# Kernel tuning notes

Measured on AMD Instinct MI355X. Metric: run time of the kernel, lower is better.

Reference implementation:

```python
import jax, jax.numpy as jnp
import numpy as np

C = 256      # n_embd
H = 16       # n_head
HS = C // H  # head_size = 16
B = 64
T = 256      # <= block_size
LN_EPS = 1e-5


def _layer_norm(x, g, b):
    mu = jnp.mean(x, axis=-1, keepdims=True)
    var = jnp.mean((x - mu) ** 2, axis=-1, keepdims=True)
    return (x - mu) * jax.lax.rsqrt(var + LN_EPS) * g + b


def setup_inputs() -> dict:
    key = jax.random.key(0)
    ks = jax.random.split(key, 10)
    s_in = 1.0 / np.sqrt(C)
    s_ff = 1.0 / np.sqrt(4 * C)
    return {
        "x": jax.random.normal(ks[0], (B, T, C), dtype=jnp.float32),
        # per-head Q/K/V weights, stacked: [H, C, HS] (no bias, as in Head)
        "Wq": jax.random.normal(ks[1], (H, C, HS), dtype=jnp.float32) * s_in,
        "Wk": jax.random.normal(ks[2], (H, C, HS), dtype=jnp.float32) * s_in,
        "Wv": jax.random.normal(ks[3], (H, C, HS), dtype=jnp.float32) * s_in,
        "Wp": jax.random.normal(ks[4], (C, C), dtype=jnp.float32) * s_in,
        "bp": jnp.zeros((C,), dtype=jnp.float32),
        "W1": jax.random.normal(ks[5], (C, 4 * C), dtype=jnp.float32) * s_in,
        "b1": jnp.zeros((4 * C,), dtype=jnp.float32),
        "W2": jax.random.normal(ks[6], (4 * C, C), dtype=jnp.float32) * s_ff,
        "b2": jnp.zeros((C,), dtype=jnp.float32),
        "g1": jnp.ones((C,), dtype=jnp.float32),
        "be1": jnp.zeros((C,), dtype=jnp.float32),
        "g2": jnp.ones((C,), dtype=jnp.float32),
        "be2": jnp.zeros((C,), dtype=jnp.float32),
    }


def reference(x, Wq, Wk, Wv, Wp, bp, W1, b1, W2, b2, g1, be1, g2, be2):
    Bx, Tx, Cx = x.shape
    h = _layer_norm(x, g1, be1)
    # per-head projections: [B, H, T, HS]
    q = jnp.einsum('btc,hcd->bhtd', h, Wq)
    k = jnp.einsum('btc,hcd->bhtd', h, Wk)
    v = jnp.einsum('btc,hcd->bhtd', h, Wv)
    # NOTE: original scales by C**-0.5 with C = n_embd, NOT head_size
    scale = 1.0 / np.sqrt(Cx)
    scores = jnp.einsum('bhtd,bhsd->bhts', q, k) * scale
    causal = jnp.tril(jnp.ones((Tx, Tx), dtype=bool))
    scores = jnp.where(causal, scores, -jnp.inf)
    wei = jax.nn.softmax(scores, axis=-1)  # dropout = identity (eval)
    attn = jnp.einsum('bhts,bhsd->bhtd', wei, v)
    # concat heads in order -> [B, T, C]
    attn = attn.transpose(0, 2, 1, 3).reshape(Bx, Tx, Cx)
    attn = attn @ Wp + bp
    x = x + attn
    h2 = _layer_norm(x, g2, be2)
    ffn = jax.nn.gelu(h2 @ W1 + b1, approximate=False) @ W2 + b2
    return x + ffn


if __name__ == "__main__":
    out = reference(**setup_inputs())
    print(out.shape, out.dtype)
```

## Files before the change

kernel.cpp:

```cpp
#include <hip/hip_runtime.h>
#include <hip/hip_bf16.h>

typedef __attribute__((ext_vector_type(8))) short short8;
typedef __attribute__((ext_vector_type(4))) float f32x4;
typedef __attribute__((ext_vector_type(16))) float f32x16;

__device__ __forceinline__ unsigned short f2bf(float f) {
    unsigned u = __float_as_uint(f);
    unsigned r = (u + 0x7fffu + ((u >> 16) & 1u)) >> 16;
    return (unsigned short)r;
}

__device__ __forceinline__ float fast_gelu(float v) {
    float y  = 0.7978845608f * v * (1.0f + 0.044715f * v * v);
    float ay = fabsf(y);
    float e  = __expf(2.0f * ay);
    float th = 1.0f - 2.0f / (e + 1.0f);
    th = __builtin_copysignf(th, y);
    return 0.5f * v * (1.0f + th);
}

__device__ __forceinline__ void gload16(const unsigned short* g, unsigned short* l) {
    __builtin_amdgcn_global_load_lds(
        (const __attribute__((address_space(1))) unsigned int*)g,
        (__attribute__((address_space(3))) unsigned int*)l,
        16, 0, 0);
}

__global__ __launch_bounds__(256) void prep_ln1(
    const float* __restrict__ Wq, const float* __restrict__ Wk,
    const float* __restrict__ Wv, const float* __restrict__ Wp,
    const float* __restrict__ W1, const float* __restrict__ W2,
    unsigned short* __restrict__ WqkvT, unsigned short* __restrict__ WpT,
    unsigned short* __restrict__ W1T, unsigned short* __restrict__ W2T,
    const float* __restrict__ xin, const float* __restrict__ gw,
    const float* __restrict__ bw, unsigned short* __restrict__ h1)
{
    __shared__ float smem[4096];
    const int bid = blockIdx.x, t = threadIdx.x;
    if (bid >= 624) {
        int row  = (bid - 624) * 4 + (t >> 6);
        int lane = t & 63;
        const float4 v = *reinterpret_cast<const float4*>(xin + (size_t)row * 256 + lane * 4);
        float s  = v.x + v.y + v.z + v.w;
        float sq = v.x*v.x + v.y*v.y + v.z*v.z + v.w*v.w;
#pragma unroll
        for (int m = 1; m < 64; m <<= 1) { s += __shfl_xor(s, m); sq += __shfl_xor(sq, m); }
        float mean = s * (1.0f/256.0f);
        float var  = sq * (1.0f/256.0f) - mean*mean;
        float rstd = rsqrtf(var + 1e-5f);
        const float4 g4 = *reinterpret_cast<const float4*>(gw + lane*4);
        const float4 b4 = *reinterpret_cast<const float4*>(bw + lane*4);
        ushort4 o;
        o.x = f2bf((v.x-mean)*rstd*g4.x + b4.x);
        o.y = f2bf((v.y-mean)*rstd*g4.y + b4.y);
        o.z = f2bf((v.z-mean)*rstd*g4.z + b4.z);
        o.w = f2bf((v.w-mean)*rstd*g4.w + b4.w);
        *reinterpret_cast<ushort4*>(h1 + (size_t)row*256 + lane*4) = o;
        return;
    }
    if (bid < 576) {
        const float* W; unsigned short* WT; int N, K, tile0;
        if (bid < 64)       { W = Wp; WT = WpT; N = 256;  K = 256;  tile0 = bid; }
        else if (bid < 320) { W = W1; WT = W1T; N = 1024; K = 256;  tile0 = bid - 64; }
        else                { W = W2; WT = W2T; N = 256;  K = 1024; tile0 = bid - 320; }
        int ntx = N >> 5;
        int bx = tile0 % ntx, by = tile0 / ntx;
        int c0 = bx*32, r0 = by*32;
        int tx = t & 31, ty = t >> 5;
#pragma unroll
        for (int i = 0; i < 4; ++i)
            smem[(ty + i*8)*33 + tx] = W[(size_t)(r0 + ty + i*8)*N + c0 + tx];
        __syncthreads();
#pragma unroll
        for (int i = 0; i < 4; ++i)
            WT[(size_t)(c0 + ty + i*8)*K + r0 + tx] = f2bf(smem[tx*33 + ty + i*8]);
    } else {
        int pb = bid - 576;
        int proj = pb >> 4, hh = pb & 15;
        const float* W = (proj == 0) ? Wq : ((proj == 1) ? Wk : Wv);
        float scale = (proj == 0) ? 0.0625f : 1.0f;
        const float4* src = reinterpret_cast<const float4*>(W + hh*4096);
#pragma unroll
        for (int i = 0; i < 4; ++i) {
            float4 v4 = src[t + i*256];
            *reinterpret_cast<float4*>(&smem[(t + i*256)*4]) = v4;
        }
        __syncthreads();
        int d = t >> 4, cp = (t & 15) * 16;
        unsigned short obuf[16];
#pragma unroll
        for (int i = 0; i < 16; ++i)
            obuf[i] = f2bf(smem[(cp + i)*16 + d] * scale);
        unsigned short* dst = WqkvT + (size_t)(proj*256 + hh*16 + d)*256 + cp;
        *reinterpret_cast<ushort4*>(dst)      = *reinterpret_cast<ushort4*>(&obuf[0]);
        *reinterpret_cast<ushort4*>(dst + 4)  = *reinterpret_cast<ushort4*>(&obuf[4]);
        *reinterpret_cast<ushort4*>(dst + 8)  = *reinterpret_cast<ushort4*>(&obuf[8]);
        *reinterpret_cast<ushort4*>(dst + 12) = *reinterpret_cast<ushort4*>(&obuf[12]);
    }
}

template<int NBX>
__device__ __forceinline__ void swz_bid(int& bx, int& by) {
    int nwg = gridDim.x;
    int bid = blockIdx.x;
    int vid = (bid & 7) * (nwg >> 3) + (bid >> 3);
    bx = vid % NBX;
    by = vid / NBX;
}

template<int BM, int BN, int K>
__device__ __forceinline__ void gemm_core(
    const unsigned short* __restrict__ A, const unsigned short* __restrict__ BT,
    int bx, int by, f32x4 (&acc)[BM/32][BN/32])
{
    constexpr int FM = BM/32, FN = BN/32, NT = K/32;
    __shared__ unsigned short As[2][BM*32];
    __shared__ unsigned short Bs[2][BN*32];
    const int tid = threadIdx.x, lane = tid & 63, wid = tid >> 6;
    const int wr = (wid >> 1) * (BM/2), wc = (wid & 1) * (BN/2);
    const int c16 = lane & 15, g16 = lane >> 4;
    const int lr = lane >> 2, lq = lane & 3;

#pragma unroll
    for (int m = 0; m < FM; ++m)
#pragma unroll
        for (int n = 0; n < FN; ++n) acc[m][n] = f32x4{0.f, 0.f, 0.f, 0.f};

    const unsigned short* a0 = A  + (size_t)(by*BM + lr)*K + lq*8;
    const unsigned short* b0 = BT + (size_t)(bx*BN + lr)*K + lq*8;

    auto stage = [&](int buf, int t) {
        int k0 = t * 32;
#pragma unroll
        for (int i = 0; i < BM/64; ++i) {
            int ch = wid*(BM/64) + i;
            gload16(a0 + (size_t)ch*16*K + k0, &As[buf][ch*512]);
        }
#pragma unroll
        for (int i = 0; i < BN/64; ++i) {
            int ch = wid*(BN/64) + i;
            gload16(b0 + (size_t)ch*16*K + k0, &Bs[buf][ch*512]);
        }
    };

    auto compute = [&](int buf) {
        short8 af[FM], bf[FN];
#pragma unroll
        for (int m = 0; m < FM; ++m)
            af[m] = *reinterpret_cast<const short8*>(&As[buf][(wr + m*16 + c16)*32 + g16*8]);
#pragma unroll
        for (int n = 0; n < FN; ++n)
            bf[n] = *reinterpret_cast<const short8*>(&Bs[buf][(wc + n*16 + c16)*32 + g16*8]);
#pragma unroll
        for (int m = 0; m < FM; ++m)
#pragma unroll
            for (int n = 0; n < FN; ++n)
                acc[m][n] = __builtin_amdgcn_mfma_f32_16x16x32_bf16(af[m], bf[n], acc[m][n], 0, 0, 0);
    };

    stage(0, 0);
    __syncthreads();
    int cur = 0;
    for (int t = 0; t < NT-1; ++t) {
        stage(cur ^ 1, t + 1);
        compute(cur);
        __syncthreads();
        cur ^= 1;
    }
    compute(cur);
}

template<int BM, int BN, int K>
__device__ __forceinline__ void gemm_core8(
    const unsigned short* __restrict__ A, const unsigned short* __restrict__ BT,
    int by, f32x4 (&acc)[BM/32][BN/64])
{
    constexpr int FM = BM/32, FN = BN/64, NT = K/32;
    constexpr int NCHA = BM/16, NCH = BM/16 + BN/16;
    constexpr int NR = (NCH + 7) / 8;
    __shared__ unsigned short As[2][BM*32];
    __shared__ unsigned short Bs[2][BN*32];
    const int tid = threadIdx.x, lane = tid & 63, wid = tid >> 6;
    const int wm = wid >> 2, wn = wid & 3;
    const int c16 = lane & 15, g16 = lane >> 4;
    const int lr = lane >> 2, lq = lane & 3;

#pragma unroll
    for (int m = 0; m < FM; ++m)
#pragma unroll
        for (int n = 0; n < FN; ++n) acc[m][n] = f32x4{0.f, 0.f, 0.f, 0.f};

    const unsigned short* a0 = A  + (size_t)(by*BM + lr)*K + lq*8;
    const unsigned short* b0 = BT + (size_t)lr*K + lq*8;

    auto stage = [&](int buf, int t) {
        int k0 = t * 32;
#pragma unroll
        for (int i = 0; i < NR; ++i) {
            int ch = i*8 + wid;
            if (ch < NCHA)
                gload16(a0 + (size_t)ch*16*K + k0, &As[buf][ch*512]);
            else if (ch < NCH)
                gload16(b0 + (size_t)(ch-NCHA)*16*K + k0, &Bs[buf][(ch-NCHA)*512]);
        }
    };

    auto compute = [&](int buf) {
        short8 af[FM], bf[FN];
#pragma unroll
        for (int m = 0; m < FM; ++m)
            af[m] = *reinterpret_cast<const short8*>(&As[buf][(wm*(BM/2) + m*16 + c16)*32 + g16*8]);
#pragma unroll
        for (int n = 0; n < FN; ++n)
            bf[n] = *reinterpret_cast<const short8*>(&Bs[buf][(wn*(BN/4) + n*16 + c16)*32 + g16*8]);
#pragma unroll
        for (int m = 0; m < FM; ++m)
#pragma unroll
            for (int n = 0; n < FN; ++n)
                acc[m][n] = __builtin_amdgcn_mfma_f32_16x16x32_bf16(af[m], bf[n], acc[m][n], 0, 0, 0);
    };

    stage(0, 0);
    __syncthreads();
    int cur = 0;
    for (int t = 0; t < NT-1; ++t) {
        stage(cur ^ 1, t + 1);
        compute(cur);
        __syncthreads();
        cur ^= 1;
    }
    compute(cur);
}

__global__ __launch_bounds__(256) void gemm_qkv(
    const unsigned short* __restrict__ A, const unsigned short* __restrict__ BT,
    unsigned short* __restrict__ qb, unsigned short* __restrict__ kb,
    unsigned short* __restrict__ vtb)
{
    int bx, by; swz_bid<6>(bx, by);
    f32x4 acc[4][4];
    gemm_core<128, 128, 256>(A, BT, bx, by, acc);
    const int lane = threadIdx.x & 63, wid = threadIdx.x >> 6;
    const int c16 = lane & 15, g16 = lane >> 4;
    const int wr = (wid >> 1) * 64, wc = (wid & 1) * 64;
#pragma unroll
    for (int m = 0; m < 4; ++m)
#pragma unroll
    for (int n = 0; n < 4; ++n)
#pragma unroll
    for (int j = 0; j < 4; ++j) {
        int row = by*128 + wr + m*16 + g16*4 + j;
        int col = bx*128 + wc + n*16 + c16;
        int proj = col >> 8, hh = (col >> 4) & 15, dd = col & 15;
        int b = row >> 8, t = row & 255;
        unsigned short val = f2bf(acc[m][n][j]);
        size_t bh = (size_t)(b*16 + hh);
        if (proj == 0)      qb[(bh*256 + t)*16 + dd] = val;
        else if (proj == 1) kb[(bh*256 + t)*16 + dd] = val;
        else                vtb[(bh*16 + dd)*256 + t] = val;
    }
}

__global__ __launch_bounds__(512) void gemm_wp_ln(
    const unsigned short* __restrict__ A, const unsigned short* __restrict__ BT,
    const float* __restrict__ bp, const float* __restrict__ x,
    const float* __restrict__ g2, const float* __restrict__ be2,
    float* __restrict__ x2, unsigned short* __restrict__ h2)
{
    int bx, by; swz_bid<1>(bx, by);
    f32x4 acc[2][4];
    gemm_core8<64, 256, 256>(A, BT, by, acc);

    __shared__ float rs[64][4];
    __shared__ float rq[64][4];
    const int tid = threadIdx.x, lane = tid & 63, wid = tid >> 6;
    const int c16 = lane & 15, g16 = lane >> 4;
    const int wm = wid >> 2, wn = wid & 3;

    float vv[2][4][4];
#pragma unroll
    for (int m = 0; m < 2; ++m)
#pragma unroll
    for (int n = 0; n < 4; ++n)
#pragma unroll
    for (int j = 0; j < 4; ++j) {
        int row = by*64 + wm*32 + m*16 + g16*4 + j;
        int col = wn*64 + n*16 + c16;
        size_t idx = (size_t)row*256 + col;
        float v = acc[m][n][j] + bp[col] + x[idx];
        vv[m][n][j] = v;
        x2[idx] = v;
    }
#pragma unroll
    for (int m = 0; m < 2; ++m)
#pragma unroll
    for (int j = 0; j < 4; ++j) {
        float ps = vv[m][0][j] + vv[m][1][j] + vv[m][2][j] + vv[m][3][j];
        float pq = vv[m][0][j]*vv[m][0][j] + vv[m][1][j]*vv[m][1][j]
                 + vv[m][2][j]*vv[m][2][j] + vv[m][3][j]*vv[m][3][j];
#pragma unroll
        for (int mask = 1; mask < 16; mask <<= 1) {
            ps += __shfl_xor(ps, mask);
            pq += __shfl_xor(pq, mask);
        }
        if (c16 == 0) {
            int r = wm*32 + m*16 + g16*4 + j;
            rs[r][wn] = ps;
            rq[r][wn] = pq;
        }
    }
    __syncthreads();
#pragma unroll
    for (int m = 0; m < 2; ++m)
#pragma unroll
    for (int j = 0; j < 4; ++j) {
        int r = wm*32 + m*16 + g16*4 + j;
        float s = rs[r][0] + rs[r][1] + rs[r][2] + rs[r][3];
        float q = rq[r][0] + rq[r][1] + rq[r][2] + rq[r][3];
        float mean = s * (1.0f/256.0f);
        float var  = q * (1.0f/256.0f) - mean*mean;
        float rstd = rsqrtf(var + 1e-5f);
        int row = by*64 + r;
#pragma unroll
        for (int n = 0; n < 4; ++n) {
            int col = wn*64 + n*16 + c16;
            h2[(size_t)row*256 + col] = f2bf((vv[m][n][j]-mean)*rstd*g2[col] + be2[col]);
        }
    }
}

__global__ __launch_bounds__(256) void gemm_ffn1(
    const unsigned short* __restrict__ A, const unsigned short* __restrict__ BT,
    const float* __restrict__ b1, unsigned short* __restrict__ ffh)
{
    int bx, by; swz_bid<8>(bx, by);
    f32x4 acc[4][4];
    gemm_core<128, 128, 256>(A, BT, bx, by, acc);
    const int lane = threadIdx.x & 63, wid = threadIdx.x >> 6;
    const int c16 = lane & 15, g16 = lane >> 4;
    const int wr = (wid >> 1) * 64, wc = (wid & 1) * 64;
#pragma unroll
    for (int m = 0; m < 4; ++m)
#pragma unroll
    for (int n = 0; n < 4; ++n)
#pragma unroll
    for (int j = 0; j < 4; ++j) {
        int row = by*128 + wr + m*16 + g16*4 + j;
        int col = bx*128 + wc + n*16 + c16;
        float v = acc[m][n][j] + b1[col];
        ffh[(size_t)row*1024 + col] = f2bf(fast_gelu(v));
    }
}

__global__ __launch_bounds__(512) void gemm_ffn2(
    const unsigned short* __restrict__ A, const unsigned short* __restrict__ BT,
    const float* __restrict__ b2, const float* __restrict__ x2, float* __restrict__ out)
{
    int bx, by; swz_bid<1>(bx, by);
    f32x4 acc[2][4];
    gemm_core8<64, 256, 1024>(A, BT, by, acc);
    const int lane = threadIdx.x & 63, wid = threadIdx.x >> 6;
    const int c16 = lane & 15, g16 = lane >> 4;
    const int wm = wid >> 2, wn = wid & 3;
#pragma unroll
    for (int m = 0; m < 2; ++m)
#pragma unroll
    for (int n = 0; n < 4; ++n)
#pragma unroll
    for (int j = 0; j < 4; ++j) {
        int row = by*64 + wm*32 + m*16 + g16*4 + j;
        int col = wn*64 + n*16 + c16;
        size_t idx = (size_t)row*256 + col;
        out[idx] = acc[m][n][j] + b2[col] + x2[idx];
    }
}

__global__ __launch_bounds__(256) void attn_kernel(
    const unsigned short* __restrict__ qb, const unsigned short* __restrict__ kb,
    const unsigned short* __restrict__ vtb, unsigned short* __restrict__ ao)
{
    const int bid  = blockIdx.x;
    const int half = bid & 1, h = (bid >> 1) & 15, b = bid >> 5;
    const int tid  = threadIdx.x;
    const int w    = tid >> 6, lane = tid & 63;
    const int l31  = lane & 31, hi = lane >> 5;
    const int chunk = half*4 + w;
    const int t0    = chunk * 32;
    const unsigned short* qh = qb  + (size_t)(b*16 + h) * 4096;
    const unsigned short* kh = kb  + (size_t)(b*16 + h) * 4096;
    const unsigned short* vh = vtb + (size_t)(b*16 + h) * 4096;

    short8 qf = *reinterpret_cast<const short8*>(qh + (size_t)(t0 + l31)*16 + hi*8);

    f32x16 zf, pv;
#pragma unroll
    for (int i = 0; i < 16; ++i) { zf[i] = 0.f; pv[i] = 0.f; }
    float sum = 0.f;
    const int dref = l31 & 15;

    for (int tt = 0; tt <= chunk; ++tt) {
        short8 kf = *reinterpret_cast<const short8*>(kh + (size_t)(tt*32 + l31)*16 + hi*8);
        f32x16 S = __builtin_amdgcn_mfma_f32_32x32x16_bf16(kf, qf, zf, 0, 0, 0);

        float p[16];
#pragma unroll
        for (int r = 0; r < 16; ++r) {
            float pe = __expf(S[r]);
            if (tt == chunk) {
                int s_local = (r & 3) + 8*(r >> 2) + 4*hi;
                pe = (s_local <= l31) ? pe : 0.f;
            }
            p[r] = pe;
            sum += pe;
        }

        unsigned qd[8], xd[8];
#pragma unroll
        for (int i = 0; i < 8; ++i) {
            unsigned rr;
            asm("v_cvt_pk_bf16_f32 %0, %1, %2" : "=v"(rr) : "v"(p[2*i]), "v"(p[2*i+1]));
            qd[i] = rr;
        }
#pragma unroll
        for (int i = 0; i < 8; ++i) xd[i] = (unsigned)__shfl_xor((int)qd[i], 32);

        int4 flo, fhi;
        flo.x = hi ? (int)xd[2] : (int)qd[0];
        flo.y = hi ? (int)xd[3] : (int)qd[1];
        flo.z = hi ? (int)qd[2] : (int)xd[0];
        flo.w = hi ? (int)qd[3] : (int)xd[1];
        fhi.x = hi ? (int)xd[6] : (int)qd[4];
        fhi.y = hi ? (int)xd[7] : (int)qd[5];
        fhi.z = hi ? (int)qd[6] : (int)xd[4];
        fhi.w = hi ? (int)qd[7] : (int)xd[5];
        short8 plo = __builtin_bit_cast(short8, flo);
        short8 phi = __builtin_bit_cast(short8, fhi);

        short8 vf0 = *reinterpret_cast<const short8*>(vh + (size_t)dref*256 + tt*32 + hi*8);
        short8 vf1 = *reinterpret_cast<const short8*>(vh + (size_t)dref*256 + tt*32 + 16 + hi*8);
        pv = __builtin_amdgcn_mfma_f32_32x32x16_bf16(vf0, plo, pv, 0, 0, 0);
        pv = __builtin_amdgcn_mfma_f32_32x32x16_bf16(vf1, phi, pv, 0, 0, 0);
    }

    sum += __shfl_xor(sum, 32);
    float rinv = 1.0f / sum;

    unsigned o0, o1, o2, o3;
    {
        float a0 = pv[0]*rinv, a1 = pv[1]*rinv, a2 = pv[2]*rinv, a3 = pv[3]*rinv;
        float a4 = pv[4]*rinv, a5 = pv[5]*rinv, a6 = pv[6]*rinv, a7 = pv[7]*rinv;
        asm("v_cvt_pk_bf16_f32 %0, %1, %2" : "=v"(o0) : "v"(a0), "v"(a1));
        asm("v_cvt_pk_bf16_f32 %0, %1, %2" : "=v"(o1) : "v"(a2), "v"(a3));
        asm("v_cvt_pk_bf16_f32 %0, %1, %2" : "=v"(o2) : "v"(a4), "v"(a5));
        asm("v_cvt_pk_bf16_f32 %0, %1, %2" : "=v"(o3) : "v"(a6), "v"(a7));
    }
    unsigned short* orow = ao + (size_t)(b*256 + t0 + l31)*256 + h*16;
    uint2 s01 = {o0, o1}, s23 = {o2, o3};
    *reinterpret_cast<uint2*>(orow + hi*4)     = s01;
    *reinterpret_cast<uint2*>(orow + 8 + hi*4) = s23;
}

extern "C" void kernel_launch(void* const* d_in, const int* in_sizes, int n_in,
                              void* d_out, int out_size, void* d_ws, size_t ws_size,
                              hipStream_t stream)
{
    const float* x   = (const float*)d_in[0];
    const float* Wq  = (const float*)d_in[1];
    const float* Wk  = (const float*)d_in[2];
    const float* Wv  = (const float*)d_in[3];
    const float* Wp  = (const float*)d_in[4];
    const float* bp  = (const float*)d_in[5];
    const float* W1  = (const float*)d_in[6];
    const float* b1  = (const float*)d_in[7];
    const float* W2  = (const float*)d_in[8];
    const float* b2  = (const float*)d_in[9];
    const float* g1  = (const float*)d_in[10];
    const float* be1 = (const float*)d_in[11];
    const float* g2  = (const float*)d_in[12];
    const float* be2 = (const float*)d_in[13];
    float* out = (float*)d_out;

    char* ws = (char*)d_ws;
    unsigned short* h1    = (unsigned short*)(ws);
    unsigned short* WqkvT = (unsigned short*)(ws +  8388608);
    unsigned short* WpT   = (unsigned short*)(ws +  8781824);
    unsigned short* W1T   = (unsigned short*)(ws +  8912896);
    unsigned short* W2T   = (unsigned short*)(ws +  9437184);
    unsigned short* qb    = (unsigned short*)(ws +  9961472);
    unsigned short* kb    = (unsigned short*)(ws + 18350080);
    unsigned short* vtb   = (unsigned short*)(ws + 26738688);
    unsigned short* ao    = (unsigned short*)(ws + 35127296);
    unsigned short* ffh   = qb;
    float*          x2    = (float*)(ws + 43515904);
    unsigned short* h2    = (unsigned short*)(ws + 60293120);

    prep_ln1<<<4720, 256, 0, stream>>>(Wq, Wk, Wv, Wp, W1, W2,
                                       WqkvT, WpT, W1T, W2T, x, g1, be1, h1);
    gemm_qkv<<<768, 256, 0, stream>>>(h1, WqkvT, qb, kb, vtb);
    attn_kernel<<<2048, 256, 0, stream>>>(qb, kb, vtb, ao);
    gemm_wp_ln<<<256, 512, 0, stream>>>(ao, WpT, bp, x, g2, be2, x2, h2);
    gemm_ffn1<<<1024, 256, 0, stream>>>(h2, W1T, b1, ffh);
    gemm_ffn2<<<256, 512, 0, stream>>>(ffh, W2T, b2, x2, out);
}
```

Baseline: 115.4 us.

## Fuse FFN up-projection, GELU and down-projection into one kernel

Merges the two FFN GEMM kernels into one kernel. Each 64-row block computes the 1024-wide hidden activation in four 256-column chunks, applies bias and GELU, and keeps each chunk in swizzled shared memory. It then accumulates that chunk's down-projection contribution directly. This removes the global round trip for the 16384x1024 bf16 hidden tensor and one kernel launch. In exchange, the fused kernel runs only 256 blocks, each doing all the up-projection work serially, with more shared memory per block and many barriers, so parallelism and occupancy for the first GEMM drop sharply.

```diff
diff --git a/kernel.cpp b/kernel.cpp
--- a/kernel.cpp
+++ b/kernel.cpp
@@ -330,39 +330,131 @@
     }
 }
 
-__global__ __launch_bounds__(256) void gemm_ffn1(
-    const unsigned short* __restrict__ A, const unsigned short* __restrict__ BT,
-    const float* __restrict__ b1, unsigned short* __restrict__ ffh)
-{
-    int bx, by; swz_bid<8>(bx, by);
-    f32x4 acc[4][4];
-    gemm_core<128, 128, 256>(A, BT, bx, by, acc);
-    const int lane = threadIdx.x & 63, wid = threadIdx.x >> 6;
+__global__ __launch_bounds__(512) void gemm_ffn_fused(
+    const unsigned short* __restrict__ h2, const unsigned short* __restrict__ W1T,
+    const unsigned short* __restrict__ W2T, const float* __restrict__ b1,
+    const float* __restrict__ b2, const float* __restrict__ x2,
+    float* __restrict__ out)
+{
+    __shared__ unsigned short hid[64*256];
+    __shared__ unsigned short As[2][64*32];
+    __shared__ unsigned short Bs[2][256*32];
+    char* hidb = (char*)hid;
+
+    int bx_, by; swz_bid<1>(bx_, by);
+    const int tid = threadIdx.x, lane = tid & 63, wid = tid >> 6;
+    const int wm = wid >> 2, wn = wid & 3;
     const int c16 = lane & 15, g16 = lane >> 4;
-    const int wr = (wid >> 1) * 64, wc = (wid & 1) * 64;
-#pragma unroll
-    for (int m = 0; m < 4; ++m)
-#pragma unroll
-    for (int n = 0; n < 4; ++n)
-#pragma unroll
-    for (int j = 0; j < 4; ++j) {
-        int row = by*128 + wr + m*16 + g16*4 + j;
-        int col = bx*128 + wc + n*16 + c16;
-        float v = acc[m][n][j] + b1[col];
-        ffh[(size_t)row*1024 + col] = f2bf(fast_gelu(v));
-    }
-}
-
-__global__ __launch_bounds__(512) void gemm_ffn2(
-    const unsigned short* __restrict__ A, const unsigned short* __restrict__ BT,
-    const float* __restrict__ b2, const float* __restrict__ x2, float* __restrict__ out)
-{
-    int bx, by; swz_bid<1>(bx, by);
-    f32x4 acc[2][4];
-    gemm_core8<64, 256, 1024>(A, BT, by, acc);
-    const int lane = threadIdx.x & 63, wid = threadIdx.x >> 6;
-    const int c16 = lane & 15, g16 = lane >> 4;
-    const int wm = wid >> 2, wn = wid & 3;
+    const int lr = lane >> 2, lq = lane & 3;
+
+    const unsigned short* a0 = h2 + (size_t)(by*64 + lr)*256 + lq*8;
+
+    f32x4 oacc[2][4];
+#pragma unroll
+    for (int m = 0; m < 2; ++m)
+#pragma unroll
+        for (int n = 0; n < 4; ++n) oacc[m][n] = f32x4{0.f, 0.f, 0.f, 0.f};
+
+    for (int hc = 0; hc < 4; ++hc) {
+        const unsigned short* b0 = W1T + (size_t)(hc*256 + lr)*256 + lq*8;
+        f32x4 pacc[2][4];
+#pragma unroll
+        for (int m = 0; m < 2; ++m)
+#pragma unroll
+            for (int n = 0; n < 4; ++n) pacc[m][n] = f32x4{0.f, 0.f, 0.f, 0.f};
+
+        auto stage1 = [&](int buf, int t) {
+            int k0 = t * 32;
+#pragma unroll
+            for (int i = 0; i < 3; ++i) {
+                int ch = i*8 + wid;
+                if (ch < 4)
+                    gload16(a0 + (size_t)ch*16*256 + k0, &As[buf][ch*512]);
+                else if (ch < 20)
+                    gload16(b0 + (size_t)(ch-4)*16*256 + k0, &Bs[buf][(ch-4)*512]);
+            }
+        };
+        auto compute1 = [&](int buf) {
+            short8 af[2], bf[4];
+#pragma unroll
+            for (int m = 0; m < 2; ++m)
+                af[m] = *reinterpret_cast<const short8*>(&As[buf][(wm*32 + m*16 + c16)*32 + g16*8]);
+#pragma unroll
+            for (int n = 0; n < 4; ++n)
+                bf[n] = *reinterpret_cast<const short8*>(&Bs[buf][(wn*64 + n*16 + c16)*32 + g16*8]);
+#pragma unroll
+            for (int m = 0; m < 2; ++m)
+#pragma unroll
+                for (int n = 0; n < 4; ++n)
+                    pacc[m][n] = __builtin_amdgcn_mfma_f32_16x16x32_bf16(af[m], bf[n], pacc[m][n], 0, 0, 0);
+        };
+
+        stage1(0, 0);
+        __syncthreads();
+        int cur = 0;
+        for (int t = 0; t < 7; ++t) {
+            stage1(cur ^ 1, t + 1);
+            compute1(cur);
+            __syncthreads();
+            cur ^= 1;
+        }
+        compute1(cur);
+        __syncthreads();
+
+#pragma unroll
+        for (int m = 0; m < 2; ++m)
+#pragma unroll
+        for (int n = 0; n < 4; ++n)
+#pragma unroll
+        for (int j = 0; j < 4; ++j) {
+            int rl = wm*32 + m*16 + g16*4 + j;
+            int cl = wn*64 + n*16 + c16;
+            float v = pacc[m][n][j] + b1[hc*256 + cl];
+            unsigned short g = f2bf(fast_gelu(v));
+            *(unsigned short*)(hidb + rl*512 + ((cl*2) ^ ((rl & 7) << 4))) = g;
+        }
+        __syncthreads();
+
+        const unsigned short* b20 = W2T + (size_t)lr*1024 + hc*256 + lq*8;
+        auto stage2 = [&](int buf, int kk) {
+            int k0 = kk * 32;
+#pragma unroll
+            for (int i = 0; i < 2; ++i) {
+                int ch = i*8 + wid;
+                gload16(b20 + (size_t)ch*16*1024 + k0, &Bs[buf][ch*512]);
+            }
+        };
+        auto compute2 = [&](int buf, int kk) {
+            short8 af[2], bf[4];
+#pragma unroll
+            for (int m = 0; m < 2; ++m) {
+                int rl = wm*32 + m*16 + c16;
+                int cb = (kk*32 + g16*8) * 2;
+                af[m] = *reinterpret_cast<const short8*>(hidb + rl*512 + (cb ^ ((rl & 7) << 4)));
+            }
+#pragma unroll
+            for (int n = 0; n < 4; ++n)
+                bf[n] = *reinterpret_cast<const short8*>(&Bs[buf][(wn*64 + n*16 + c16)*32 + g16*8]);
+#pragma unroll
+            for (int m = 0; m < 2; ++m)
+#pragma unroll
+                for (int n = 0; n < 4; ++n)
+                    oacc[m][n] = __builtin_amdgcn_mfma_f32_16x16x32_bf16(af[m], bf[n], oacc[m][n], 0, 0, 0);
+        };
+
+        stage2(0, 0);
+        __syncthreads();
+        cur = 0;
+        for (int kk = 0; kk < 7; ++kk) {
+            stage2(cur ^ 1, kk + 1);
+            compute2(cur, kk);
+            __syncthreads();
+            cur ^= 1;
+        }
+        compute2(cur, 7);
+        __syncthreads();
+    }
+
 #pragma unroll
     for (int m = 0; m < 2; ++m)
 #pragma unroll
@@ -372,7 +464,7 @@
         int row = by*64 + wm*32 + m*16 + g16*4 + j;
         int col = wn*64 + n*16 + c16;
         size_t idx = (size_t)row*256 + col;
-        out[idx] = acc[m][n][j] + b2[col] + x2[idx];
+        out[idx] = oacc[m][n][j] + b2[col] + x2[idx];
     }
 }
 
@@ -491,7 +583,6 @@
     unsigned short* kb    = (unsigned short*)(ws + 18350080);
     unsigned short* vtb   = (unsigned short*)(ws + 26738688);
     unsigned short* ao    = (unsigned short*)(ws + 35127296);
-    unsigned short* ffh   = qb;
     float*          x2    = (float*)(ws + 43515904);
     unsigned short* h2    = (unsigned short*)(ws + 60293120);
 
@@ -500,6 +591,5 @@
     gemm_qkv<<<768, 256, 0, stream>>>(h1, WqkvT, qb, kb, vtb);
     attn_kernel<<<2048, 256, 0, stream>>>(qb, kb, vtb, ao);
     gemm_wp_ln<<<256, 512, 0, stream>>>(ao, WpT, bp, x, g2, be2, x2, h2);
-    gemm_ffn1<<<1024, 256, 0, stream>>>(h2, W1T, b1, ffh);
-    gemm_ffn2<<<256, 512, 0, stream>>>(ffh, W2T, b2, x2, out);
-}
+    gemm_ffn_fused<<<256, 512, 0, stream>>>(h2, W1T, W2T, b1, b2, x2, out);
+}
```

After: 118.6 us. +2.8%, slower.
